# Optimization experiments

Hardware: AMD Instinct MI355X
Metric: run time of the kernel (lower is better)

## Reference

```python
import jax, jax.numpy as jnp
import numpy as np

OUT, IN = 4096, 4096
B, S = 4, 2048


def setup_inputs() -> dict:
    key = jax.random.key(0)
    k_x, k_wh, k_wm, k_wl, k_r, k_s, k_b = jax.random.split(key, 7)
    x = jax.random.normal(k_x, (B, S, IN), dtype=jnp.float32)
    r = jax.random.uniform(k_r, (OUT, IN))
    high_mask = r < 0.2
    medium_mask = (r < 0.5) & ~high_mask
    weight_high = jax.random.normal(k_wh, (OUT, IN), dtype=jnp.float32) * 0.02 * high_mask
    weight_medium = (jax.random.normal(k_wm, (OUT, IN), dtype=jnp.float32) * 0.02 * medium_mask).astype(jnp.float16)
    weight_low = jax.random.randint(k_wl, (OUT, IN), -127, 128, dtype=jnp.int32)
    low_scale = jax.random.uniform(k_s, (1,), dtype=jnp.float32) * 0.001 + 1e-4
    bias = jax.random.normal(k_b, (OUT,), dtype=jnp.float32) * 0.02
    return {
        "x": x,
        "weight_high": weight_high,
        "weight_medium": weight_medium,
        "weight_low": weight_low,
        "high_precision_mask": high_mask,
        "medium_precision_mask": medium_mask,
        "low_scale": low_scale,
        "bias": bias,
    }


def reference(x, weight_high, weight_medium, weight_low,
              high_precision_mask, medium_precision_mask, low_scale, bias):
    # Reconstruct full fp32 weight from three precision tiers (as in forward).
    low_mask = ~high_precision_mask & ~medium_precision_mask
    w = (weight_high
         + medium_precision_mask * weight_medium.astype(jnp.float32)
         + low_mask * (weight_low.astype(jnp.float32) * low_scale[0]))
    # F.linear: x @ w.T + bias ; [B,S,IN] x [OUT,IN] -> [B,S,OUT]
    return jnp.einsum('bsi,oi->bso', x, w) + bias
```

## Files before the change

kernel.cpp:

```cpp
#include <hip/hip_runtime.h>
#include <hip/hip_bf16.h>
#include <hip/hip_fp16.h>


#define M_DIM 8192
#define N_DIM 4096
#define K_DIM 4096

typedef __attribute__((ext_vector_type(8))) short short8;
typedef __attribute__((ext_vector_type(4))) float floatx4;
typedef __attribute__((ext_vector_type(8))) _Float16 half8;
typedef __attribute__((ext_vector_type(8))) unsigned char uchar8;
typedef __attribute__((ext_vector_type(4))) int intx4;

__device__ inline unsigned short f2bf(float f) {
    union { float f; unsigned u; } v; v.f = f;
    return (unsigned short)((v.u + 0x7fffu + ((v.u >> 16) & 1u)) >> 16);
}

__device__ inline void async16(const void* g, const void* l) {
    __builtin_amdgcn_global_load_lds(
        (const __attribute__((address_space(1))) void*)g,
        (__attribute__((address_space(3))) void*)l,
        16, 0, 0);
}

__global__ __launch_bounds__(256) void prep_kernel(
        const float* __restrict__ x,
        const float* __restrict__ wh, const void* __restrict__ wm_raw,
        const int* __restrict__ wl, const void* __restrict__ hm_raw,
        const void* __restrict__ mm_raw, const float* __restrict__ scale_p,
        unsigned short* __restrict__ wbf, unsigned short* __restrict__ xbf) {
    const int bid = blockIdx.x;
    const int tid = threadIdx.x;

    if (bid >= 8192) {
        const size_t i = ((size_t)(bid - 8192) * 256 + tid) * 8;
        floatx4 f0 = *(const floatx4*)(x + i);
        floatx4 f1 = *(const floatx4*)(x + i + 4);
        short8 s;
        s[0] = (short)f2bf(f0[0]); s[1] = (short)f2bf(f0[1]);
        s[2] = (short)f2bf(f0[2]); s[3] = (short)f2bf(f0[3]);
        s[4] = (short)f2bf(f1[0]); s[5] = (short)f2bf(f1[1]);
        s[6] = (short)f2bf(f1[2]); s[7] = (short)f2bf(f1[3]);
        *(short8*)(xbf + i) = s;
        return;
    }

    const int lane = tid & 63;
    union { unsigned u; float f; } pw; pw.u = ((const unsigned*)wm_raw)[lane];
    const float pav = fabsf(pw.f);
    const bool wm_f32  = __popcll(__ballot(pav > 1e-4f && pav < 1.0f)) >= 4;
    const bool mask_u8 = __ballot(((const unsigned*)hm_raw)[lane] > 1u) != 0;

    const size_t i = ((size_t)bid * 256 + tid) * 8;
    const float scale = *scale_p;

    floatx4 h0 = *(const floatx4*)(wh + i);
    floatx4 h1 = *(const floatx4*)(wh + i + 4);
    intx4  l0 = *(const intx4*)(wl + i);
    intx4  l1 = *(const intx4*)(wl + i + 4);

    float mv[8];
    if (wm_f32) {
        floatx4 m0 = *(const floatx4*)((const float*)wm_raw + i);
        floatx4 m1 = *(const floatx4*)((const float*)wm_raw + i + 4);
#pragma unroll
        for (int e = 0; e < 4; ++e) { mv[e] = m0[e]; mv[e + 4] = m1[e]; }
    } else {
        half8 m = *(const half8*)((const _Float16*)wm_raw + i);
#pragma unroll
        for (int e = 0; e < 8; ++e) mv[e] = (float)m[e];
    }

    int lowmask[8];
    if (mask_u8) {
        uchar8 a = *(const uchar8*)((const unsigned char*)hm_raw + i);
        uchar8 b = *(const uchar8*)((const unsigned char*)mm_raw + i);
#pragma unroll
        for (int e = 0; e < 8; ++e) lowmask[e] = (a[e] | b[e]) == 0;
    } else {
        intx4 a0 = *(const intx4*)((const int*)hm_raw + i);
        intx4 a1 = *(const intx4*)((const int*)hm_raw + i + 4);
        intx4 b0 = *(const intx4*)((const int*)mm_raw + i);
        intx4 b1 = *(const intx4*)((const int*)mm_raw + i + 4);
#pragma unroll
        for (int e = 0; e < 4; ++e) {
            lowmask[e]     = (a0[e] | b0[e]) == 0;
            lowmask[e + 4] = (a1[e] | b1[e]) == 0;
        }
    }

    short8 s;
#pragma unroll
    for (int e = 0; e < 8; ++e) {
        float v = (e < 4 ? h0[e] : h1[e - 4]) + mv[e];
        int   lw = (e < 4 ? l0[e] : l1[e - 4]);
        if (lowmask[e]) v += (float)lw * scale;
        s[e] = (short)f2bf(v);
    }
    *(short8*)(wbf + i) = s;
}

__global__ __launch_bounds__(512, 2) void gemm256_kernel(
        const unsigned short* __restrict__ A,
        const unsigned short* __restrict__ Bw,
        const float* __restrict__ bias,
        float* __restrict__ out) {
    extern __shared__ char smem[];
    const int tid  = threadIdx.x;
    const int wave = tid >> 6, lane = tid & 63;
    const int lrow = lane & 15, lquad = lane >> 4;

    const int wg  = blockIdx.x;
    const int swz = (wg & 7) * 64 + (wg >> 3);
    const int bm0 = (swz >> 4) * 256;
    const int bn0 = (swz & 15) * 256;

    const int wr = wave >> 2, wc = wave & 3;
    const int wm = wr * 128, wn = wc * 64;

    const int lane2 = lane ^ ((lane & 32) ? 2 : 0);
    const int srow  = wave * 16 + (lane2 >> 2);
    const int scol  = (lane2 & 3) * 8;
    const unsigned short* gA0 = A  + (size_t)(bm0 + srow) * K_DIM + scol;
    const unsigned short* gA1 = gA0 + (size_t)128 * K_DIM;
    const unsigned short* gB0 = Bw + (size_t)(bn0 + srow) * K_DIM + scol;
    const unsigned short* gB1 = gB0 + (size_t)128 * K_DIM;
    const int dstA = wave * 1024;

    int offA[8], offB[4];
#pragma unroll
    for (int i = 0; i < 8; ++i) {
        int q = (wm + i * 16 + lrow) * 64 + lquad * 16;
        offA[i] = q ^ (((q >> 9) & 1) << 5);
    }
#pragma unroll
    for (int j = 0; j < 4; ++j) {
        int q = (wn + j * 16 + lrow) * 64 + lquad * 16;
        offB[j] = 16384 + (q ^ (((q >> 9) & 1) << 5));
    }

    floatx4 acc[8][4] = {};

#define STAGEF(TILE) do { \
        char* d_ = smem + ((TILE) & 3) * 32768 + dstA; \
        const unsigned ko_ = (unsigned)(TILE) * 32u; \
        async16(gA0 + ko_, d_); async16(gA1 + ko_, d_ + 8192); \
        async16(gB0 + ko_, d_ + 16384); async16(gB1 + ko_, d_ + 24576); } while (0)

#define WAITV(n) asm volatile("s_waitcnt vmcnt(" #n ")" ::: "memory")
#define BAR() do { __builtin_amdgcn_s_barrier(); asm volatile("" ::: "memory"); } while (0)
#define LGKM0() asm volatile("s_waitcnt lgkmcnt(0)" ::: "memory")
#define SCHED0() __builtin_amdgcn_sched_barrier(0)

#define PHASES(T, DO_STAGE) do { \
        const char* ab_ = smem + ((T) & 3) * 32768; \
        const unsigned ko3_ = ((unsigned)(T) + 3u) * 32u; \
        short8 af_[4], bq_[4], ag_[4]; \
        _Pragma("unroll") \
        for (int i_ = 0; i_ < 4; ++i_) af_[i_] = *(const short8*)(ab_ + offA[i_]); \
        _Pragma("unroll") \
        for (int j_ = 0; j_ < 4; ++j_) bq_[j_] = *(const short8*)(ab_ + offB[j_]); \
        if (DO_STAGE) { char* d_ = smem + (((T) + 3) & 3) * 32768 + dstA; \
            async16(gA0 + ko3_, d_); async16(gA1 + ko3_, d_ + 8192); } \
        SCHED0(); \
        BAR(); \
        LGKM0(); \
        SCHED0(); \
        __builtin_amdgcn_s_setprio(1); \
        _Pragma("unroll") \
        for (int i_ = 0; i_ < 4; ++i_) \
            _Pragma("unroll") \
            for (int j_ = 0; j_ < 4; ++j_) \
                acc[i_][j_] = __builtin_amdgcn_mfma_f32_16x16x32_bf16(af_[i_], bq_[j_], acc[i_][j_], 0, 0, 0); \
        __builtin_amdgcn_s_setprio(0); \
        _Pragma("unroll") \
        for (int i_ = 0; i_ < 4; ++i_) ag_[i_] = *(const short8*)(ab_ + offA[4 + i_]); \
        if (DO_STAGE) { char* d_ = smem + (((T) + 3) & 3) * 32768 + dstA; \
            async16(gB0 + ko3_, d_ + 16384); async16(gB1 + ko3_, d_ + 24576); } \
        SCHED0(); \
        BAR(); \
        LGKM0(); \
        SCHED0(); \
        __builtin_amdgcn_s_setprio(1); \
        _Pragma("unroll") \
        for (int i_ = 0; i_ < 4; ++i_) \
            _Pragma("unroll") \
            for (int j_ = 0; j_ < 4; ++j_) \
                acc[4 + i_][j_] = __builtin_amdgcn_mfma_f32_16x16x32_bf16(ag_[i_], bq_[j_], acc[4 + i_][j_], 0, 0, 0); \
        __builtin_amdgcn_s_setprio(0); \
    } while (0)

    STAGEF(0); STAGEF(1); STAGEF(2);

    const int NT = K_DIM / 32;
    for (int t = 0; t < NT - 3; ++t) {
        WAITV(8);
        BAR();
        PHASES(t, true);
    }
    WAITV(8); BAR(); PHASES(NT - 3, false);
    WAITV(4); BAR(); PHASES(NT - 2, false);
    WAITV(0); BAR(); PHASES(NT - 1, false);

#undef STAGEF
#undef PHASES
#undef WAITV
#undef BAR
#undef LGKM0
#undef SCHED0

#pragma unroll
    for (int j = 0; j < 4; ++j) {
        const int col = bn0 + wn + j * 16 + lrow;
        const float bv = bias[col];
#pragma unroll
        for (int i = 0; i < 8; ++i) {
            const int row = bm0 + wm + i * 16 + lquad * 4;
#pragma unroll
            for (int r = 0; r < 4; ++r)
                out[(size_t)(row + r) * N_DIM + col] = acc[i][j][r] + bv;
        }
    }
}

__global__ __launch_bounds__(256) void gemm_fused_kernel(
        const float* __restrict__ X,
        const unsigned short* __restrict__ Bw,
        const float* __restrict__ bias,
        float* __restrict__ out) {
    __shared__ unsigned short As[128 * 32];
    __shared__ unsigned short Bs[128 * 32];
    const int tid  = threadIdx.x;
    const int wave = tid >> 6, lane = tid & 63;
    const int bm0 = blockIdx.y * 128, bn0 = blockIdx.x * 128;
    const int wm = (wave >> 1) * 64, wn = (wave & 1) * 64;
    const int lrow = lane & 15, lquad = lane >> 4;
    const int arow = tid >> 1, acol = (tid & 1) * 16;

    floatx4 acc[4][4] = {};

    for (int k0 = 0; k0 < K_DIM; k0 += 32) {
        __syncthreads();
#pragma unroll
        for (int c = 0; c < 2; ++c) {
            const int lb  = wave * 2048 + c * 1024;
            const int e   = (lb >> 1) + lane * 8;
            const int row = e >> 5, col = e & 31;
            async16(Bw + (size_t)(bn0 + row) * K_DIM + k0 + col, (const char*)Bs + lb);
        }
        {
            const float* g = X + (size_t)(bm0 + arow) * K_DIM + k0 + acol;
            floatx4 f0 = *(const floatx4*)(g);
            floatx4 f1 = *(const floatx4*)(g + 4);
            floatx4 f2 = *(const floatx4*)(g + 8);
            floatx4 f3 = *(const floatx4*)(g + 12);
            short8 s0, s1;
            s0[0]=(short)f2bf(f0[0]); s0[1]=(short)f2bf(f0[1]); s0[2]=(short)f2bf(f0[2]); s0[3]=(short)f2bf(f0[3]);
            s0[4]=(short)f2bf(f1[0]); s0[5]=(short)f2bf(f1[1]); s0[6]=(short)f2bf(f1[2]); s0[7]=(short)f2bf(f1[3]);
            s1[0]=(short)f2bf(f2[0]); s1[1]=(short)f2bf(f2[1]); s1[2]=(short)f2bf(f2[2]); s1[3]=(short)f2bf(f2[3]);
            s1[4]=(short)f2bf(f3[0]); s1[5]=(short)f2bf(f3[1]); s1[6]=(short)f2bf(f3[2]); s1[7]=(short)f2bf(f3[3]);
            *(short8*)&As[arow * 32 + acol]     = s0;
            *(short8*)&As[arow * 32 + acol + 8] = s1;
        }
        __syncthreads();

        short8 af[4], bf[4];
#pragma unroll
        for (int i = 0; i < 4; ++i)
            af[i] = *(const short8*)&As[(wm + i * 16 + lrow) * 32 + lquad * 8];
#pragma unroll
        for (int j = 0; j < 4; ++j)
            bf[j] = *(const short8*)&Bs[(wn + j * 16 + lrow) * 32 + lquad * 8];
#pragma unroll
        for (int i = 0; i < 4; ++i)
#pragma unroll
            for (int j = 0; j < 4; ++j)
                acc[i][j] = __builtin_amdgcn_mfma_f32_16x16x32_bf16(af[i], bf[j], acc[i][j], 0, 0, 0);
    }

#pragma unroll
    for (int j = 0; j < 4; ++j) {
        const int col = bn0 + wn + j * 16 + lrow;
        const float bv = bias[col];
#pragma unroll
        for (int i = 0; i < 4; ++i) {
            const int row = bm0 + wm + i * 16 + lquad * 4;
#pragma unroll
            for (int r = 0; r < 4; ++r)
                out[(size_t)(row + r) * N_DIM + col] = acc[i][j][r] + bv;
        }
    }
}

extern "C" void kernel_launch(void* const* d_in, const int* in_sizes, int n_in,
                              void* d_out, int out_size, void* d_ws, size_t ws_size,
                              hipStream_t stream) {
    const float*    x     = (const float*)d_in[0];
    const float*    wh    = (const float*)d_in[1];
    const void*     wmed  = d_in[2];
    const int*      wl    = (const int*)d_in[3];
    const void*     hm    = d_in[4];
    const void*     mm    = d_in[5];
    const float*    scale = (const float*)d_in[6];
    const float*    bias  = (const float*)d_in[7];
    float*          out   = (float*)d_out;

    unsigned short* wbf   = (unsigned short*)((char*)d_ws + 256);
    unsigned short* xbf   = (unsigned short*)((char*)d_ws + 256 + (size_t)N_DIM * K_DIM * 2);
    const size_t need_full = 256 + (size_t)N_DIM * K_DIM * 2 + (size_t)M_DIM * K_DIM * 2;

    static bool attr_done = false;
    if (!attr_done) {
        (void)hipFuncSetAttribute(reinterpret_cast<const void*>(gemm256_kernel),
                                  hipFuncAttributeMaxDynamicSharedMemorySize, 131072);
        attr_done = true;
    }

    if (ws_size >= need_full) {
        prep_kernel<<<24576, 256, 0, stream>>>(x, wh, wmed, wl, hm, mm, scale, wbf, xbf);
        gemm256_kernel<<<dim3(512), dim3(512), 131072, stream>>>(xbf, wbf, bias, out);
    } else {
        prep_kernel<<<8192, 256, 0, stream>>>(x, wh, wmed, wl, hm, mm, scale, wbf, wbf);
        dim3 grid(N_DIM / 128, M_DIM / 128);
        gemm_fused_kernel<<<grid, 256, 0, stream>>>(x, wbf, bias, out);
    }
}
```

Baseline: 675.1 us.

## Load A fragments directly from global into registers, stage only B in LDS

```diff
diff --git a/kernel.cpp b/kernel.cpp
--- a/kernel.cpp
+++ b/kernel.cpp
@@ -123,93 +123,83 @@
     const int lane2 = lane ^ ((lane & 32) ? 2 : 0);
     const int srow  = wave * 16 + (lane2 >> 2);
     const int scol  = (lane2 & 3) * 8;
-    const unsigned short* gA0 = A  + (size_t)(bm0 + srow) * K_DIM + scol;
-    const unsigned short* gA1 = gA0 + (size_t)128 * K_DIM;
     const unsigned short* gB0 = Bw + (size_t)(bn0 + srow) * K_DIM + scol;
     const unsigned short* gB1 = gB0 + (size_t)128 * K_DIM;
-    const int dstA = wave * 1024;
-
-    int offA[8], offB[4];
-#pragma unroll
-    for (int i = 0; i < 8; ++i) {
-        int q = (wm + i * 16 + lrow) * 64 + lquad * 16;
-        offA[i] = q ^ (((q >> 9) & 1) << 5);
-    }
+    const int dstB = wave * 1024;
+
+    int offB[4];
 #pragma unroll
     for (int j = 0; j < 4; ++j) {
         int q = (wn + j * 16 + lrow) * 64 + lquad * 16;
-        offB[j] = 16384 + (q ^ (((q >> 9) & 1) << 5));
-    }
+        offB[j] = q ^ (((q >> 9) & 1) << 5);
+    }
+
+    const unsigned short* pa = A + (size_t)(bm0 + wm + lrow) * K_DIM + lquad * 8;
 
     floatx4 acc[8][4] = {};
-
-#define STAGEF(TILE) do { \
-        char* d_ = smem + ((TILE) & 3) * 32768 + dstA; \
-        const unsigned ko_ = (unsigned)(TILE) * 32u; \
-        async16(gA0 + ko_, d_); async16(gA1 + ko_, d_ + 8192); \
-        async16(gB0 + ko_, d_ + 16384); async16(gB1 + ko_, d_ + 24576); } while (0)
+    short8 afX[8], afY[8];
+    short8 bq[4];
+
+#define APREF(AF, T) do { \
+        _Pragma("unroll") \
+        for (int i_ = 0; i_ < 8; ++i_) \
+            AF[i_] = *(const short8*)(pa + (size_t)i_ * 16 * K_DIM + (size_t)(T) * 32); \
+    } while (0)
+
+#define BSTAGE(T) do { \
+        char* d_ = smem + ((T) & 3) * 16384 + dstB; \
+        const unsigned ko_ = (unsigned)(T) * 32u; \
+        async16(gB0 + ko_, d_); async16(gB1 + ko_, d_ + 8192); } while (0)
+
+#define BREAD(T) do { \
+        const char* b_ = smem + ((T) & 3) * 16384; \
+        _Pragma("unroll") \
+        for (int j_ = 0; j_ < 4; ++j_) bq[j_] = *(const short8*)(b_ + offB[j_]); \
+    } while (0)
+
+#define MMA(AF) do { \
+        __builtin_amdgcn_s_setprio(1); \
+        _Pragma("unroll") \
+        for (int i_ = 0; i_ < 8; ++i_) \
+            _Pragma("unroll") \
+            for (int j_ = 0; j_ < 4; ++j_) \
+                acc[i_][j_] = __builtin_amdgcn_mfma_f32_16x16x32_bf16(AF[i_], bq[j_], acc[i_][j_], 0, 0, 0); \
+        __builtin_amdgcn_s_setprio(0); } while (0)
 
 #define WAITV(n) asm volatile("s_waitcnt vmcnt(" #n ")" ::: "memory")
 #define BAR() do { __builtin_amdgcn_s_barrier(); asm volatile("" ::: "memory"); } while (0)
-#define LGKM0() asm volatile("s_waitcnt lgkmcnt(0)" ::: "memory")
 #define SCHED0() __builtin_amdgcn_sched_barrier(0)
 
-#define PHASES(T, DO_STAGE) do { \
-        const char* ab_ = smem + ((T) & 3) * 32768; \
-        const unsigned ko3_ = ((unsigned)(T) + 3u) * 32u; \
-        short8 af_[4], bq_[4], ag_[4]; \
-        _Pragma("unroll") \
-        for (int i_ = 0; i_ < 4; ++i_) af_[i_] = *(const short8*)(ab_ + offA[i_]); \
-        _Pragma("unroll") \
-        for (int j_ = 0; j_ < 4; ++j_) bq_[j_] = *(const short8*)(ab_ + offB[j_]); \
-        if (DO_STAGE) { char* d_ = smem + (((T) + 3) & 3) * 32768 + dstA; \
-            async16(gA0 + ko3_, d_); async16(gA1 + ko3_, d_ + 8192); } \
+#define ITER(T, AFC, AFN, DOB) do { \
+        WAITV(2); \
+        BAR(); \
+        BREAD(T); \
+        APREF(AFN, (T) + 1); \
+        if (DOB) BSTAGE((T) + 3); \
         SCHED0(); \
-        BAR(); \
-        LGKM0(); \
-        SCHED0(); \
-        __builtin_amdgcn_s_setprio(1); \
-        _Pragma("unroll") \
-        for (int i_ = 0; i_ < 4; ++i_) \
-            _Pragma("unroll") \
-            for (int j_ = 0; j_ < 4; ++j_) \
-                acc[i_][j_] = __builtin_amdgcn_mfma_f32_16x16x32_bf16(af_[i_], bq_[j_], acc[i_][j_], 0, 0, 0); \
-        __builtin_amdgcn_s_setprio(0); \
-        _Pragma("unroll") \
-        for (int i_ = 0; i_ < 4; ++i_) ag_[i_] = *(const short8*)(ab_ + offA[4 + i_]); \
-        if (DO_STAGE) { char* d_ = smem + (((T) + 3) & 3) * 32768 + dstA; \
-            async16(gB0 + ko3_, d_ + 16384); async16(gB1 + ko3_, d_ + 24576); } \
-        SCHED0(); \
-        BAR(); \
-        LGKM0(); \
-        SCHED0(); \
-        __builtin_amdgcn_s_setprio(1); \
-        _Pragma("unroll") \
-        for (int i_ = 0; i_ < 4; ++i_) \
-            _Pragma("unroll") \
-            for (int j_ = 0; j_ < 4; ++j_) \
-                acc[4 + i_][j_] = __builtin_amdgcn_mfma_f32_16x16x32_bf16(ag_[i_], bq_[j_], acc[4 + i_][j_], 0, 0, 0); \
-        __builtin_amdgcn_s_setprio(0); \
-    } while (0)
-
-    STAGEF(0); STAGEF(1); STAGEF(2);
+        MMA(AFC); } while (0)
+
+    APREF(afX, 0);
+    BSTAGE(0); BSTAGE(1); BSTAGE(2);
 
     const int NT = K_DIM / 32;
-    for (int t = 0; t < NT - 3; ++t) {
-        WAITV(8);
-        BAR();
-        PHASES(t, true);
-    }
-    WAITV(8); BAR(); PHASES(NT - 3, false);
-    WAITV(4); BAR(); PHASES(NT - 2, false);
-    WAITV(0); BAR(); PHASES(NT - 1, false);
-
-#undef STAGEF
-#undef PHASES
+    for (int t = 0; t < NT - 4; t += 2) {
+        ITER(t,     afX, afY, true);
+        ITER(t + 1, afY, afX, true);
+    }
+    ITER(NT - 4, afX, afY, true);
+    ITER(NT - 3, afY, afX, false);
+    WAITV(0); BAR(); BREAD(NT - 2); APREF(afY, NT - 1); SCHED0(); MMA(afX);
+    WAITV(0); BAR(); BREAD(NT - 1); SCHED0(); MMA(afY);
+
+#undef APREF
+#undef BSTAGE
+#undef BREAD
+#undef MMA
 #undef WAITV
 #undef BAR
-#undef LGKM0
 #undef SCHED0
+#undef ITER
 
 #pragma unroll
     for (int j = 0; j < 4; ++j) {
@@ -314,13 +304,13 @@
     static bool attr_done = false;
     if (!attr_done) {
         (void)hipFuncSetAttribute(reinterpret_cast<const void*>(gemm256_kernel),
-                                  hipFuncAttributeMaxDynamicSharedMemorySize, 131072);
+                                  hipFuncAttributeMaxDynamicSharedMemorySize, 65536);
         attr_done = true;
     }
 
     if (ws_size >= need_full) {
         prep_kernel<<<24576, 256, 0, stream>>>(x, wh, wmed, wl, hm, mm, scale, wbf, xbf);
-        gemm256_kernel<<<dim3(512), dim3(512), 131072, stream>>>(xbf, wbf, bias, out);
+        gemm256_kernel<<<dim3(512), dim3(512), 65536, stream>>>(xbf, wbf, bias, out);
     } else {
         prep_kernel<<<8192, 256, 0, stream>>>(x, wh, wmed, wl, hm, mm, scale, wbf, wbf);
         dim3 grid(N_DIM / 128, M_DIM / 128);
```

Measured after the change: 1.044 ms. 1.55x slower.

## Double-buffer LDS fragments in registers and use one barrier per K-tile

Applied to the files above, without the earlier changes.

```diff
diff --git a/kernel.cpp b/kernel.cpp
--- a/kernel.cpp
+++ b/kernel.cpp
@@ -127,7 +127,7 @@
     const unsigned short* gA1 = gA0 + (size_t)128 * K_DIM;
     const unsigned short* gB0 = Bw + (size_t)(bn0 + srow) * K_DIM + scol;
     const unsigned short* gB1 = gB0 + (size_t)128 * K_DIM;
-    const int dstA = wave * 1024;
+    const int dstS = wave * 1024;
 
     int offA[8], offB[4];
 #pragma unroll
@@ -142,74 +142,68 @@
     }
 
     floatx4 acc[8][4] = {};
-
-#define STAGEF(TILE) do { \
-        char* d_ = smem + ((TILE) & 3) * 32768 + dstA; \
-        const unsigned ko_ = (unsigned)(TILE) * 32u; \
+    short8 afX[8], bqX[4], afY[8], bqY[4];
+
+#define STAGE(T) do { \
+        char* d_ = smem + ((T) & 3) * 32768 + dstS; \
+        const unsigned ko_ = (unsigned)(T) * 32u; \
         async16(gA0 + ko_, d_); async16(gA1 + ko_, d_ + 8192); \
         async16(gB0 + ko_, d_ + 16384); async16(gB1 + ko_, d_ + 24576); } while (0)
 
-#define WAITV(n) asm volatile("s_waitcnt vmcnt(" #n ")" ::: "memory")
-#define BAR() do { __builtin_amdgcn_s_barrier(); asm volatile("" ::: "memory"); } while (0)
-#define LGKM0() asm volatile("s_waitcnt lgkmcnt(0)" ::: "memory")
-#define SCHED0() __builtin_amdgcn_sched_barrier(0)
-
-#define PHASES(T, DO_STAGE) do { \
+#define RDS(AF, BQ, T) do { \
         const char* ab_ = smem + ((T) & 3) * 32768; \
-        const unsigned ko3_ = ((unsigned)(T) + 3u) * 32u; \
-        short8 af_[4], bq_[4], ag_[4]; \
         _Pragma("unroll") \
-        for (int i_ = 0; i_ < 4; ++i_) af_[i_] = *(const short8*)(ab_ + offA[i_]); \
+        for (int i_ = 0; i_ < 8; ++i_) AF[i_] = *(const short8*)(ab_ + offA[i_]); \
         _Pragma("unroll") \
-        for (int j_ = 0; j_ < 4; ++j_) bq_[j_] = *(const short8*)(ab_ + offB[j_]); \
-        if (DO_STAGE) { char* d_ = smem + (((T) + 3) & 3) * 32768 + dstA; \
-            async16(gA0 + ko3_, d_); async16(gA1 + ko3_, d_ + 8192); } \
-        SCHED0(); \
-        BAR(); \
-        LGKM0(); \
-        SCHED0(); \
+        for (int j_ = 0; j_ < 4; ++j_) BQ[j_] = *(const short8*)(ab_ + offB[j_]); \
+    } while (0)
+
+#define MMA(AF, BQ) do { \
         __builtin_amdgcn_s_setprio(1); \
         _Pragma("unroll") \
-        for (int i_ = 0; i_ < 4; ++i_) \
+        for (int i_ = 0; i_ < 8; ++i_) \
             _Pragma("unroll") \
             for (int j_ = 0; j_ < 4; ++j_) \
-                acc[i_][j_] = __builtin_amdgcn_mfma_f32_16x16x32_bf16(af_[i_], bq_[j_], acc[i_][j_], 0, 0, 0); \
-        __builtin_amdgcn_s_setprio(0); \
-        _Pragma("unroll") \
-        for (int i_ = 0; i_ < 4; ++i_) ag_[i_] = *(const short8*)(ab_ + offA[4 + i_]); \
-        if (DO_STAGE) { char* d_ = smem + (((T) + 3) & 3) * 32768 + dstA; \
-            async16(gB0 + ko3_, d_ + 16384); async16(gB1 + ko3_, d_ + 24576); } \
+                acc[i_][j_] = __builtin_amdgcn_mfma_f32_16x16x32_bf16(AF[i_], BQ[j_], acc[i_][j_], 0, 0, 0); \
+        __builtin_amdgcn_s_setprio(0); } while (0)
+
+#define WAITV(n) asm volatile("s_waitcnt vmcnt(" #n ")" ::: "memory")
+#define LGKM(n)  asm volatile("s_waitcnt lgkmcnt(" #n ")" ::: "memory")
+#define BAR() do { __builtin_amdgcn_s_barrier(); asm volatile("" ::: "memory"); } while (0)
+#define SCHED0() __builtin_amdgcn_sched_barrier(0)
+
+#define ITER(T, AFC, BQC, AFN, BQN, DOB) do { \
+        WAITV(4); \
+        BAR(); \
+        if (DOB) STAGE((T) + 3); \
+        RDS(AFN, BQN, (T) + 1); \
+        LGKM(12); \
         SCHED0(); \
-        BAR(); \
-        LGKM0(); \
-        SCHED0(); \
-        __builtin_amdgcn_s_setprio(1); \
-        _Pragma("unroll") \
-        for (int i_ = 0; i_ < 4; ++i_) \
-            _Pragma("unroll") \
-            for (int j_ = 0; j_ < 4; ++j_) \
-                acc[4 + i_][j_] = __builtin_amdgcn_mfma_f32_16x16x32_bf16(ag_[i_], bq_[j_], acc[4 + i_][j_], 0, 0, 0); \
-        __builtin_amdgcn_s_setprio(0); \
-    } while (0)
-
-    STAGEF(0); STAGEF(1); STAGEF(2);
+        MMA(AFC, BQC); } while (0)
+
+    STAGE(0); STAGE(1); STAGE(2);
+    WAITV(8);
+    BAR();
+    RDS(afX, bqX, 0);
 
     const int NT = K_DIM / 32;
-    for (int t = 0; t < NT - 3; ++t) {
-        WAITV(8);
-        BAR();
-        PHASES(t, true);
-    }
-    WAITV(8); BAR(); PHASES(NT - 3, false);
-    WAITV(4); BAR(); PHASES(NT - 2, false);
-    WAITV(0); BAR(); PHASES(NT - 1, false);
-
-#undef STAGEF
-#undef PHASES
+    for (int t = 0; t < NT - 4; t += 2) {
+        ITER(t,     afX, bqX, afY, bqY, true);
+        ITER(t + 1, afY, bqY, afX, bqX, true);
+    }
+    ITER(NT - 4, afX, bqX, afY, bqY, true);
+    ITER(NT - 3, afY, bqY, afX, bqX, false);
+    WAITV(0); BAR(); RDS(afY, bqY, NT - 1); LGKM(12); SCHED0(); MMA(afX, bqX);
+    LGKM(0); SCHED0(); MMA(afY, bqY);
+
+#undef STAGE
+#undef RDS
+#undef MMA
 #undef WAITV
+#undef LGKM
 #undef BAR
-#undef LGKM0
 #undef SCHED0
+#undef ITER
 
 #pragma unroll
     for (int j = 0; j < 4; ++j) {
```

Result: no change. 662.6 us (-1.8%).
